# Optimization experiments

Hardware: AMD Instinct MI355X
Metric: run time of the kernel (lower is better)

## Reference

```python
import jax, jax.numpy as jnp
import numpy as np
import math

M, T, D, H, QK, K_ACT = 16, 512, 512, 512, 256, 4


def setup_inputs() -> dict:
    key = jax.random.key(0)
    ks = jax.random.split(key, 16)

    def xavier(k, shape):
        fan = shape[-1] + shape[-2]
        return jax.random.normal(k, shape, jnp.float32) * np.float32(math.sqrt(2.0 / fan))

    def bias(k, shape, fan_in):
        b = np.float32(1.0 / math.sqrt(fan_in))
        return jax.random.uniform(k, shape, jnp.float32, -b, b)

    return {
        "inputs": jax.random.normal(ks[0], (M, T, D), jnp.float32),
        # per-mechanism InputSelection params
        "Wq": xavier(ks[1], (M, QK, H)), "bq": bias(ks[2], (M, QK), H),
        "Wk": xavier(ks[3], (M, QK, D)), "bk": bias(ks[4], (M, QK), D),
        "Wv": xavier(ks[5], (M, D, D)), "bv": bias(ks[6], (M, D), D),
        # per-mechanism LSTMCell params (gate order i, f, g, o)
        "W_ih": xavier(ks[7], (M, 4 * H, D)), "b_ih": bias(ks[8], (M, 4 * H), H),
        "W_hh": xavier(ks[9], (M, 4 * H, H)), "b_hh": bias(ks[10], (M, 4 * H), H),
        # GroupLinearLayer weights for interaction attention
        "Wq_g": xavier(ks[11], (M, H, H)),
        "Wk_g": xavier(ks[12], (M, H, H)),
        "Wv_g": xavier(ks[13], (M, H, H)),
    }


def reference(inputs, Wq, bq, Wk, bk, Wv, bv, W_ih, b_ih, W_hh, b_hh, Wq_g, Wk_g, Wv_g):
    scale = 1.0 / math.sqrt(Wk.shape[1])  # 1/sqrt(key_size)
    xs = jnp.swapaxes(inputs, 0, 1)  # (T, M, D) for scan over time
    h0 = jnp.zeros((M, H), inputs.dtype)
    c0 = jnp.zeros((M, H), inputs.dtype)

    def step(carry, x_t):
        h, c = carry  # (M,H), (M,H)
        # --- InputSelection: augmented input rows are [zeros, x_t] ---
        q = jnp.einsum('mh,mqh->mq', h, Wq) + bq            # (M,QK)
        key_x = jnp.einsum('md,mkd->mk', x_t, Wk) + bk      # key of real input row
        logit0 = jnp.sum(q * bk, -1) * scale                # key of zero row == bias
        logit1 = jnp.sum(q * key_x, -1) * scale
        att = jax.nn.softmax(jnp.stack([logit0, logit1], -1), axis=-1)  # (M,2)
        val1 = jnp.einsum('md,mvd->mv', x_t, Wv) + bv       # (M,D)
        sel = att[:, 0:1] * bv + att[:, 1:2] * val1         # value of zero row == bias
        # --- top-k routing: smallest attention to the null input ---
        _, active_idx = jax.lax.top_k(-att[:, 0], K_ACT)
        mask = jnp.zeros((M,), inputs.dtype).at[active_idx].set(1.0)
        m = mask[:, None]
        # --- LSTMCell for all mechanisms, masked afterwards ---
        gates = (jnp.einsum('md,mgd->mg', sel, W_ih) + b_ih
                 + jnp.einsum('mh,mgh->mg', h, W_hh) + b_hh)  # (M,4H)
        i, f, g, o = jnp.split(gates, 4, axis=-1)
        c_new = jax.nn.sigmoid(f) * c + jax.nn.sigmoid(i) * jnp.tanh(g)
        h_new = jax.nn.sigmoid(o) * jnp.tanh(c_new)
        temp_h = m * h_new + (1 - m) * h
        new_c = m * c_new  # inactive cells are reset to zero (as in original)
        # --- interaction attention across mechanisms ---
        q2 = jnp.einsum('mh,mho->mo', temp_h, Wq_g)
        k2 = jnp.einsum('mh,mho->mo', temp_h, Wk_g)
        v2 = jnp.einsum('mh,mho->mo', temp_h, Wv_g)
        att2 = jax.nn.softmax(q2 @ k2.T, axis=1)            # (M,M), no sqrt scaling
        inter = (m * att2) @ v2                             # zero rows for inactive
        new_h = inter + (1 - m) * h + m * temp_h
        return (new_h, new_c), (new_h.reshape(-1), active_idx)

    _, (all_h, all_idx) = jax.lax.scan(step, (h0, c0), xs)
    return all_h, all_idx  # (T, M*H), (T, K_ACT)
```

## Files before the change

kernel.cpp:

```cpp
#include <hip/hip_runtime.h>

constexpr int M_ = 16, T_ = 512, D_ = 512, H_ = 512, QK_ = 256, G4_ = 2048;
constexpr float SCALE_ = 1.0f / 16.0f;

constexpr size_t KEY_OFF = 0;
constexpr size_t VAL_OFF = 2097152;
constexpr size_t H_OFF   = 6291456;
constexpr size_t C_OFF   = H_OFF + 8192;
constexpr size_t TH_OFF  = C_OFF + 8192;
constexpr size_t K2_OFF  = TH_OFF + 8192;
constexpr size_t V2_OFF  = K2_OFF + 8192;
constexpr size_t Q2_OFF  = V2_OFF + 8192;
constexpr size_t L0_OFF  = Q2_OFF + 2048;
constexpr size_t L1_OFF  = L0_OFF + 256;
constexpr size_t BAR_OFF = L1_OFF + 256;
constexpr int    BAR_WORDS = 16 * 32 + 32;

__device__ inline void load8f(const float* p, float f[8]) {
  float4 a = reinterpret_cast<const float4*>(p)[0];
  float4 b = reinterpret_cast<const float4*>(p)[1];
  f[0] = a.x; f[1] = a.y; f[2] = a.z; f[3] = a.w;
  f[4] = b.x; f[5] = b.y; f[6] = b.z; f[7] = b.w;
}

__device__ inline float waveReduce(float v) {
#pragma unroll
  for (int d = 32; d > 0; d >>= 1) v += __shfl_xor(v, d);
  return v;
}

__device__ inline float sigm(float x) { return 1.f / (1.f + expf(-x)); }

__device__ __forceinline__ void gbar(float* wsf, unsigned idx) {
  unsigned* bar = reinterpret_cast<unsigned*>(wsf + BAR_OFF);
  __syncthreads();
  if (threadIdx.x == 0) {
    __threadfence();
    const int sub = blockIdx.x >> 4;
    unsigned a = __hip_atomic_fetch_add(&bar[sub * 32], 1u, __ATOMIC_RELAXED,
                                        __HIP_MEMORY_SCOPE_AGENT);
    if (a == idx * 16u - 1u)
      __hip_atomic_fetch_add(&bar[512], 1u, __ATOMIC_RELAXED,
                             __HIP_MEMORY_SCOPE_AGENT);
    while (__hip_atomic_load(&bar[512], __ATOMIC_RELAXED,
                             __HIP_MEMORY_SCOPE_AGENT) < idx * 16u)
      __builtin_amdgcn_s_sleep(2);
    __threadfence();
  }
  __syncthreads();
}

__global__ void __launch_bounds__(256) keyval_kernel(
    const float* __restrict__ x, const float* __restrict__ Wk,
    const float* __restrict__ Wv, const float* __restrict__ bk,
    const float* __restrict__ bv, float* __restrict__ wsf) {
  __shared__ float Xs[64][33];
  __shared__ float Ws[64][33];
  int bid = blockIdx.x, tid = threadIdx.x;
  if (bid == 0) {
    for (int i = tid; i < BAR_WORDS; i += 256)
      reinterpret_cast<unsigned*>(wsf + BAR_OFF)[i] = 0u;
  }
  int m = bid / 96, r = bid % 96;
  int tt = r / 12, ot = r % 12;
  const float* xb = x + ((size_t)m * T_ + tt * 64) * D_;
  const float* wb; const float* bias; float* dst; int ld;
  if (ot < 4) {
    wb = Wk + (size_t)m * QK_ * D_ + (size_t)(ot * 64) * D_;
    bias = bk + m * QK_ + ot * 64;
    dst = wsf + KEY_OFF + ((size_t)m * T_ + tt * 64) * QK_ + ot * 64;
    ld = QK_;
  } else {
    wb = Wv + (size_t)m * D_ * D_ + (size_t)((ot - 4) * 64) * D_;
    bias = bv + m * D_ + (ot - 4) * 64;
    dst = wsf + VAL_OFF + ((size_t)m * T_ + tt * 64) * D_ + (ot - 4) * 64;
    ld = D_;
  }
  int lr = tid >> 2, lc = (tid & 3) * 8;
  int tx = tid & 15, ty = tid >> 4;
  float acc[4][4] = {};
  for (int k0 = 0; k0 < D_; k0 += 32) {
    float tmp[8];
    load8f(xb + (size_t)lr * D_ + k0 + lc, tmp);
#pragma unroll
    for (int i = 0; i < 8; ++i) Xs[lr][lc + i] = tmp[i];
    load8f(wb + (size_t)lr * D_ + k0 + lc, tmp);
#pragma unroll
    for (int i = 0; i < 8; ++i) Ws[lr][lc + i] = tmp[i];
    __syncthreads();
#pragma unroll
    for (int kk = 0; kk < 32; ++kk) {
      float xa[4], wv4[4];
#pragma unroll
      for (int a = 0; a < 4; ++a) xa[a] = Xs[ty * 4 + a][kk];
#pragma unroll
      for (int b = 0; b < 4; ++b) wv4[b] = Ws[tx * 4 + b][kk];
#pragma unroll
      for (int a = 0; a < 4; ++a)
#pragma unroll
        for (int b = 0; b < 4; ++b) acc[a][b] += xa[a] * wv4[b];
    }
    __syncthreads();
  }
#pragma unroll
  for (int b = 0; b < 4; ++b) {
    float bias_v = bias[tx * 4 + b];
#pragma unroll
    for (int a = 0; a < 4; ++a)
      dst[(size_t)(ty * 4 + a) * ld + tx * 4 + b] = acc[a][b] + bias_v;
  }
}

__global__ void __launch_bounds__(1024, 4) rim_main(
    const float* __restrict__ Wq, const float* __restrict__ bq,
    const float* __restrict__ bk, const float* __restrict__ bv,
    const float* __restrict__ Wih, const float* __restrict__ bih,
    const float* __restrict__ Whh, const float* __restrict__ bhh,
    const float* __restrict__ Wqg, const float* __restrict__ Wkg,
    const float* __restrict__ Wvg,
    float* __restrict__ wsf, float* __restrict__ out0, float* __restrict__ out1) {
  const int wg = blockIdx.x, tid = threadIdx.x;
  const int lane = tid & 63, wv = tid >> 6;
  const int m = wg >> 4, g = wg & 15;
  const int h32 = tid >> 5, oi = tid & 31;

  float* keyA = wsf + KEY_OFF;
  float* valA = wsf + VAL_OFF;
  float* hB  = wsf + H_OFF;
  float* cB  = wsf + C_OFF;
  float* thB = wsf + TH_OFF;
  float* k2B = wsf + K2_OFF;
  float* v2B = wsf + V2_OFF;
  float* q2B = wsf + Q2_OFF;
  float* l0B = wsf + L0_OFF;
  float* l1B = wsf + L1_OFF;

  __shared__ float s_newh[4][512];
  __shared__ float s_dv[512];
  __shared__ float s_pdk[16][32];
  __shared__ float s_pdv[16][32];
  __shared__ float s_pdq[16][32];
  __shared__ float s_small[64];
  __shared__ float s_w2[64];
  __shared__ float s_redA[16];
  __shared__ float s_redB[16];
  __shared__ float s_gv[4][8];

  float wqr[8], wkr[16], wvr[16];
  load8f(Wq + ((size_t)m * QK_ + g * 16 + wv) * H_ + lane * 8, wqr);
  {
    const size_t wo = ((size_t)m * H_ + h32 * 16) * H_ + g * 32 + oi;
#pragma unroll
    for (int i = 0; i < 16; ++i) wkr[i] = Wkg[wo + (size_t)i * H_];
#pragma unroll
    for (int i = 0; i < 16; ++i) wvr[i] = Wvg[wo + (size_t)i * H_];
  }
  const float qb = bq[m * QK_ + g * 16 + wv];
  const float kb = bk[m * QK_ + g * 16 + wv];

  unsigned bno = 0;

  if (g == 0 && tid < 512) {
    hB[m * 512 + tid] = 0.f;
    cB[m * 512 + tid] = 0.f;
  }
  gbar(wsf, ++bno);

  int p0 = 0, p1 = 0, p2 = 0, p3 = 0;
  int r0 = 0, r1 = 0, r2 = 0, r3 = 0;

  for (int t = 0; t <= T_; ++t) {
    int slot = -1;
    if (t > 0) {
      slot = (m == p0) ? 0 : (m == p1) ? 1 : (m == p2) ? 2 : (m == p3) ? 3 : -1;
      if (slot >= 0) {
        if (tid < 512) {
          int pr = tid >> 3, part = tid & 7;
          int s_ = pr >> 4, j_ = pr & 15;
          const float4* q4 = reinterpret_cast<const float4*>(q2B + s_ * 512 + part * 64);
          const float4* k4 = reinterpret_cast<const float4*>(k2B + j_ * 512 + part * 64);
          float acc = 0.f;
#pragma unroll
          for (int i = 0; i < 16; ++i) {
            float4 a = q4[i], b = k4[i];
            acc += a.x * b.x + a.y * b.y + a.z * b.z + a.w * b.w;
          }
          acc += __shfl_xor(acc, 1);
          acc += __shfl_xor(acc, 2);
          acc += __shfl_xor(acc, 4);
          if (part == 0) s_small[pr] = acc;
        }
        __syncthreads();
        if (tid < 4) {
          float mx = -1e30f;
          for (int j = 0; j < 16; ++j) mx = fmaxf(mx, s_small[tid * 16 + j]);
          float sm = 0.f;
          for (int j = 0; j < 16; ++j) {
            float e = expf(s_small[tid * 16 + j] - mx);
            s_w2[tid * 16 + j] = e; sm += e;
          }
          float inv = 1.f / sm;
          for (int j = 0; j < 16; ++j) s_w2[tid * 16 + j] *= inv;
        }
        __syncthreads();
        {
          int s_ = tid >> 8, o0 = (tid & 255) * 2;
          float ax = 0.f, ay = 0.f;
#pragma unroll
          for (int j = 0; j < 16; ++j) {
            float w = s_w2[s_ * 16 + j];
            float2 v = *reinterpret_cast<const float2*>(v2B + j * 512 + o0);
            ax += w * v.x; ay += w * v.y;
          }
          int myrow = s_ == 0 ? p0 : s_ == 1 ? p1 : s_ == 2 ? p2 : p3;
          const float2 th = *reinterpret_cast<const float2*>(thB + (size_t)myrow * 512 + o0);
          s_newh[s_][o0] = ax + th.x;
          s_newh[s_][o0 + 1] = ay + th.y;
        }
        __syncthreads();
      }
      if (g == 0 && tid < 512) {
        float v = (slot >= 0) ? s_newh[slot][tid] : hB[m * 512 + tid];
        out0[(size_t)(t - 1) * (M_ * H_) + m * 512 + tid] = v;
        if (slot >= 0) hB[m * 512 + tid] = v;
      }
    }
    if (t == T_) break;

    {
      float kv = keyA[((size_t)m * T_ + t) * QK_ + g * 16 + wv];
      float hreg[8];
      if (slot >= 0) {
#pragma unroll
        for (int i = 0; i < 8; ++i) hreg[i] = s_newh[slot][lane * 8 + i];
      } else {
        load8f(hB + m * 512 + lane * 8, hreg);
      }
      float acc = 0.f;
#pragma unroll
      for (int i = 0; i < 8; ++i) acc += hreg[i] * wqr[i];
      acc = waveReduce(acc);
      if (lane == 0) {
        float q = acc + qb;
        s_redA[wv] = q * kv;
        s_redB[wv] = q * kb;
      }
      __syncthreads();
      if (tid == 0) {
        float a = 0.f, b = 0.f;
        for (int w = 0; w < 16; ++w) { a += s_redA[w]; b += s_redB[w]; }
        l1B[m * 16 + g] = a;
        l0B[m * 16 + g] = b;
      }
    }
    gbar(wsf, ++bno);

    if (tid < 16) {
      float l0 = 0.f, l1 = 0.f;
      for (int i = 0; i < 16; ++i) { l0 += l0B[tid * 16 + i]; l1 += l1B[tid * 16 + i]; }
      l0 *= SCALE_; l1 *= SCALE_;
      float mx = fmaxf(l0, l1);
      float e0 = expf(l0 - mx), e1 = expf(l1 - mx);
      float inv = 1.f / (e0 + e1);
      s_small[tid] = e0 * inv;
      s_small[16 + tid] = e1 * inv;
    }
    __syncthreads();
    {
      unsigned chosen = 0;
      int rr[4];
#pragma unroll
      for (int s = 0; s < 4; ++s) {
        float best = -2.f; int bm = 0;
        for (int mm = 0; mm < 16; ++mm) {
          if (chosen & (1u << mm)) continue;
          float v = -s_small[mm];
          if (v > best) { best = v; bm = mm; }
        }
        rr[s] = bm; chosen |= 1u << bm;
      }
      r0 = rr[0]; r1 = rr[1]; r2 = rr[2]; r3 = rr[3];
    }
    if (wg == 0 && tid < 4) {
      int rowv = tid == 0 ? r0 : tid == 1 ? r1 : tid == 2 ? r2 : r3;
      out1[(size_t)t * 4 + tid] = (float)rowv;
    }
    {
      int slot_c = wg >> 6, jc = wg & 63, j0 = jc * 8;
      int mA = slot_c == 0 ? r0 : slot_c == 1 ? r1 : slot_c == 2 ? r2 : r3;
      float a0v = s_small[mA], a1v = s_small[16 + mA];
      float bvr[8], vlr[8], hr[8];
      load8f(bv + mA * D_ + lane * 8, bvr);
      load8f(valA + ((size_t)mA * T_ + t) * D_ + lane * 8, vlr);
      load8f(hB + mA * 512 + lane * 8, hr);
      float selr[8];
#pragma unroll
      for (int i = 0; i < 8; ++i) selr[i] = a0v * bvr[i] + a1v * vlr[i];
#pragma unroll
      for (int u = 0; u < 2; ++u) {
        int gl = wv * 2 + u;
        int type = gl >> 3, jj = gl & 7;
        int gidx = type * 512 + j0 + jj;
        float wi[8], wh[8];
        load8f(Wih + ((size_t)mA * G4_ + gidx) * D_ + lane * 8, wi);
        load8f(Whh + ((size_t)mA * G4_ + gidx) * H_ + lane * 8, wh);
        float acc = 0.f;
#pragma unroll
        for (int k = 0; k < 8; ++k) acc += selr[k] * wi[k] + hr[k] * wh[k];
        acc = waveReduce(acc);
        if (lane == 0)
          s_gv[type][jj] = acc + bih[mA * G4_ + gidx] + bhh[mA * G4_ + gidx];
      }
      __syncthreads();
      if (tid < 8) {
        float gi = s_gv[0][tid], gf = s_gv[1][tid], gg = s_gv[2][tid], go = s_gv[3][tid];
        int j = j0 + tid;
        float cold = cB[mA * 512 + j];
        float cn = sigm(gf) * cold + sigm(gi) * tanhf(gg);
        float hn = sigm(go) * tanhf(cn);
        cB[mA * 512 + j] = cn;
        thB[mA * 512 + j] = hn;
      }
    }
    gbar(wsf, ++bno);

    {
      unsigned amask = (1u << r0) | (1u << r1) | (1u << r2) | (1u << r3);
      unsigned pmask = (1u << p0) | (1u << p1) | (1u << p2) | (1u << p3);
      bool act = (amask >> m) & 1;
      bool prevact = (t > 0) && ((pmask >> m) & 1);
      bool dirty = act || prevact || (t == 0);
      if (dirty) {
        const float* src = act ? thB + m * 512 : hB + m * 512;
        if (tid < 512) s_dv[tid] = src[tid];
        float wq2[16];
        int qslot = -1;
        if (act) {
          qslot = (m == r0) ? 0 : (m == r1) ? 1 : (m == r2) ? 2 : 3;
          const size_t wo = ((size_t)m * H_ + h32 * 16) * H_ + g * 32 + oi;
#pragma unroll
          for (int i = 0; i < 16; ++i) wq2[i] = Wqg[wo + (size_t)i * H_];
        }
        __syncthreads();
        float pk = 0.f, pv = 0.f, pq = 0.f;
#pragma unroll
        for (int i = 0; i < 16; ++i) {
          float s = s_dv[h32 * 16 + i];
          pk += s * wkr[i];
          pv += s * wvr[i];
        }
        if (act) {
#pragma unroll
          for (int i = 0; i < 16; ++i) pq += s_dv[h32 * 16 + i] * wq2[i];
        }
        pk += __shfl_xor(pk, 32);
        pv += __shfl_xor(pv, 32);
        pq += __shfl_xor(pq, 32);
        if (lane < 32) {
          s_pdk[wv][lane] = pk;
          s_pdv[wv][lane] = pv;
          s_pdq[wv][lane] = pq;
        }
        __syncthreads();
        if (tid < 32) {
          float a = 0.f, b = 0.f, c = 0.f;
          for (int w = 0; w < 16; ++w) {
            a += s_pdk[w][tid]; b += s_pdv[w][tid]; c += s_pdq[w][tid];
          }
          k2B[m * 512 + g * 32 + tid] = a;
          v2B[m * 512 + g * 32 + tid] = b;
          if (act) q2B[qslot * 512 + g * 32 + tid] = c;
        }
      }
      if (!act && prevact && g == 0 && tid < 512) cB[m * 512 + tid] = 0.f;
    }
    p0 = r0; p1 = r1; p2 = r2; p3 = r3;
    gbar(wsf, ++bno);
  }
}

extern "C" void kernel_launch(void* const* d_in, const int* in_sizes, int n_in,
                              void* d_out, int out_size, void* d_ws, size_t ws_size,
                              hipStream_t stream) {
  const float* x   = (const float*)d_in[0];
  const float* Wq  = (const float*)d_in[1];
  const float* bq  = (const float*)d_in[2];
  const float* Wk  = (const float*)d_in[3];
  const float* bk  = (const float*)d_in[4];
  const float* Wv  = (const float*)d_in[5];
  const float* bv  = (const float*)d_in[6];
  const float* Wih = (const float*)d_in[7];
  const float* bih = (const float*)d_in[8];
  const float* Whh = (const float*)d_in[9];
  const float* bhh = (const float*)d_in[10];
  const float* Wqg = (const float*)d_in[11];
  const float* Wkg = (const float*)d_in[12];
  const float* Wvg = (const float*)d_in[13];
  float* wsf = (float*)d_ws;
  float* out0 = (float*)d_out;
  float* out1 = out0 + (size_t)T_ * M_ * H_;
  (void)in_sizes; (void)n_in; (void)out_size; (void)ws_size;

  hipLaunchKernelGGL(keyval_kernel, dim3(1536), dim3(256), 0, stream,
                     x, Wk, Wv, bk, bv, wsf);

  void* kargs[] = {(void*)&Wq, (void*)&bq, (void*)&bk, (void*)&bv,
                   (void*)&Wih, (void*)&bih, (void*)&Whh, (void*)&bhh,
                   (void*)&Wqg, (void*)&Wkg, (void*)&Wvg,
                   (void*)&wsf, (void*)&out0, (void*)&out1};
  hipLaunchCooperativeKernel((void*)rim_main, dim3(256), dim3(1024), kargs, 0,
                             stream);
}
```

Baseline: 35.69 ms.

## Replace grid barrier threadfences with agent-scope atomic loads/stores for shared state

```diff
diff --git a/kernel.cpp b/kernel.cpp
--- a/kernel.cpp
+++ b/kernel.cpp
@@ -23,6 +23,24 @@
   f[4] = b.x; f[5] = b.y; f[6] = b.z; f[7] = b.w;
 }
 
+__device__ __forceinline__ float ldf(const float* p) {
+  return __hip_atomic_load(p, __ATOMIC_RELAXED, __HIP_MEMORY_SCOPE_AGENT);
+}
+__device__ __forceinline__ void stf(float* p, float v) {
+  __hip_atomic_store(p, v, __ATOMIC_RELAXED, __HIP_MEMORY_SCOPE_AGENT);
+}
+__device__ __forceinline__ float2 ldf2(const float* p) {
+  unsigned long long u = __hip_atomic_load(
+      reinterpret_cast<const unsigned long long*>(p),
+      __ATOMIC_RELAXED, __HIP_MEMORY_SCOPE_AGENT);
+  return __builtin_bit_cast(float2, u);
+}
+__device__ __forceinline__ void ld8f_cg(const float* p, float f[8]) {
+  float2 a = ldf2(p), b = ldf2(p + 2), c = ldf2(p + 4), d = ldf2(p + 6);
+  f[0] = a.x; f[1] = a.y; f[2] = b.x; f[3] = b.y;
+  f[4] = c.x; f[5] = c.y; f[6] = d.x; f[7] = d.y;
+}
+
 __device__ inline float waveReduce(float v) {
 #pragma unroll
   for (int d = 32; d > 0; d >>= 1) v += __shfl_xor(v, d);
@@ -33,9 +51,9 @@
 
 __device__ __forceinline__ void gbar(float* wsf, unsigned idx) {
   unsigned* bar = reinterpret_cast<unsigned*>(wsf + BAR_OFF);
+  asm volatile("s_waitcnt vmcnt(0)" ::: "memory");
   __syncthreads();
   if (threadIdx.x == 0) {
-    __threadfence();
     const int sub = blockIdx.x >> 4;
     unsigned a = __hip_atomic_fetch_add(&bar[sub * 32], 1u, __ATOMIC_RELAXED,
                                         __HIP_MEMORY_SCOPE_AGENT);
@@ -44,10 +62,10 @@
                              __HIP_MEMORY_SCOPE_AGENT);
     while (__hip_atomic_load(&bar[512], __ATOMIC_RELAXED,
                              __HIP_MEMORY_SCOPE_AGENT) < idx * 16u)
-      __builtin_amdgcn_s_sleep(2);
-    __threadfence();
+      __builtin_amdgcn_s_sleep(1);
   }
   __syncthreads();
+  __builtin_amdgcn_sched_barrier(0);
 }
 
 __global__ void __launch_bounds__(256) keyval_kernel(
@@ -140,6 +158,8 @@
   __shared__ float s_pdk[16][32];
   __shared__ float s_pdv[16][32];
   __shared__ float s_pdq[16][32];
+  __shared__ float s_l0[256];
+  __shared__ float s_l1[256];
   __shared__ float s_small[64];
   __shared__ float s_w2[64];
   __shared__ float s_redA[16];
@@ -161,8 +181,8 @@
   unsigned bno = 0;
 
   if (g == 0 && tid < 512) {
-    hB[m * 512 + tid] = 0.f;
-    cB[m * 512 + tid] = 0.f;
+    stf(hB + m * 512 + tid, 0.f);
+    stf(cB + m * 512 + tid, 0.f);
   }
   gbar(wsf, ++bno);
 
@@ -177,13 +197,14 @@
         if (tid < 512) {
           int pr = tid >> 3, part = tid & 7;
           int s_ = pr >> 4, j_ = pr & 15;
-          const float4* q4 = reinterpret_cast<const float4*>(q2B + s_ * 512 + part * 64);
-          const float4* k4 = reinterpret_cast<const float4*>(k2B + j_ * 512 + part * 64);
+          const float* q4 = q2B + s_ * 512 + part * 64;
+          const float* k4 = k2B + j_ * 512 + part * 64;
           float acc = 0.f;
 #pragma unroll
           for (int i = 0; i < 16; ++i) {
-            float4 a = q4[i], b = k4[i];
-            acc += a.x * b.x + a.y * b.y + a.z * b.z + a.w * b.w;
+            float2 a0 = ldf2(q4 + i * 4), a1 = ldf2(q4 + i * 4 + 2);
+            float2 b0 = ldf2(k4 + i * 4), b1 = ldf2(k4 + i * 4 + 2);
+            acc += a0.x * b0.x + a0.y * b0.y + a1.x * b1.x + a1.y * b1.y;
           }
           acc += __shfl_xor(acc, 1);
           acc += __shfl_xor(acc, 2);
@@ -209,20 +230,20 @@
 #pragma unroll
           for (int j = 0; j < 16; ++j) {
             float w = s_w2[s_ * 16 + j];
-            float2 v = *reinterpret_cast<const float2*>(v2B + j * 512 + o0);
+            float2 v = ldf2(v2B + j * 512 + o0);
             ax += w * v.x; ay += w * v.y;
           }
           int myrow = s_ == 0 ? p0 : s_ == 1 ? p1 : s_ == 2 ? p2 : p3;
-          const float2 th = *reinterpret_cast<const float2*>(thB + (size_t)myrow * 512 + o0);
+          float2 th = ldf2(thB + (size_t)myrow * 512 + o0);
           s_newh[s_][o0] = ax + th.x;
           s_newh[s_][o0 + 1] = ay + th.y;
         }
         __syncthreads();
       }
       if (g == 0 && tid < 512) {
-        float v = (slot >= 0) ? s_newh[slot][tid] : hB[m * 512 + tid];
+        float v = (slot >= 0) ? s_newh[slot][tid] : ldf(hB + m * 512 + tid);
         out0[(size_t)(t - 1) * (M_ * H_) + m * 512 + tid] = v;
-        if (slot >= 0) hB[m * 512 + tid] = v;
+        if (slot >= 0) stf(hB + m * 512 + tid, v);
       }
     }
     if (t == T_) break;
@@ -234,7 +255,7 @@
 #pragma unroll
         for (int i = 0; i < 8; ++i) hreg[i] = s_newh[slot][lane * 8 + i];
       } else {
-        load8f(hB + m * 512 + lane * 8, hreg);
+        ld8f_cg(hB + m * 512 + lane * 8, hreg);
       }
       float acc = 0.f;
 #pragma unroll
@@ -249,15 +270,20 @@
       if (tid == 0) {
         float a = 0.f, b = 0.f;
         for (int w = 0; w < 16; ++w) { a += s_redA[w]; b += s_redB[w]; }
-        l1B[m * 16 + g] = a;
-        l0B[m * 16 + g] = b;
+        stf(l1B + m * 16 + g, a);
+        stf(l0B + m * 16 + g, b);
       }
     }
     gbar(wsf, ++bno);
 
+    if (tid < 256) {
+      s_l0[tid] = ldf(l0B + tid);
+      s_l1[tid] = ldf(l1B + tid);
+    }
+    __syncthreads();
     if (tid < 16) {
       float l0 = 0.f, l1 = 0.f;
-      for (int i = 0; i < 16; ++i) { l0 += l0B[tid * 16 + i]; l1 += l1B[tid * 16 + i]; }
+      for (int i = 0; i < 16; ++i) { l0 += s_l0[tid * 16 + i]; l1 += s_l1[tid * 16 + i]; }
       l0 *= SCALE_; l1 *= SCALE_;
       float mx = fmaxf(l0, l1);
       float e0 = expf(l0 - mx), e1 = expf(l1 - mx);
@@ -292,7 +318,7 @@
       float bvr[8], vlr[8], hr[8];
       load8f(bv + mA * D_ + lane * 8, bvr);
       load8f(valA + ((size_t)mA * T_ + t) * D_ + lane * 8, vlr);
-      load8f(hB + mA * 512 + lane * 8, hr);
+      ld8f_cg(hB + mA * 512 + lane * 8, hr);
       float selr[8];
 #pragma unroll
       for (int i = 0; i < 8; ++i) selr[i] = a0v * bvr[i] + a1v * vlr[i];
@@ -315,11 +341,11 @@
       if (tid < 8) {
         float gi = s_gv[0][tid], gf = s_gv[1][tid], gg = s_gv[2][tid], go = s_gv[3][tid];
         int j = j0 + tid;
-        float cold = cB[mA * 512 + j];
+        float cold = ldf(cB + mA * 512 + j);
         float cn = sigm(gf) * cold + sigm(gi) * tanhf(gg);
         float hn = sigm(go) * tanhf(cn);
-        cB[mA * 512 + j] = cn;
-        thB[mA * 512 + j] = hn;
+        stf(cB + mA * 512 + j, cn);
+        stf(thB + mA * 512 + j, hn);
       }
     }
     gbar(wsf, ++bno);
@@ -332,7 +358,7 @@
       bool dirty = act || prevact || (t == 0);
       if (dirty) {
         const float* src = act ? thB + m * 512 : hB + m * 512;
-        if (tid < 512) s_dv[tid] = src[tid];
+        if (tid < 512) s_dv[tid] = ldf(src + tid);
         float wq2[16];
         int qslot = -1;
         if (act) {
@@ -367,12 +393,12 @@
           for (int w = 0; w < 16; ++w) {
             a += s_pdk[w][tid]; b += s_pdv[w][tid]; c += s_pdq[w][tid];
           }
-          k2B[m * 512 + g * 32 + tid] = a;
-          v2B[m * 512 + g * 32 + tid] = b;
-          if (act) q2B[qslot * 512 + g * 32 + tid] = c;
-        }
-      }
-      if (!act && prevact && g == 0 && tid < 512) cB[m * 512 + tid] = 0.f;
+          stf(k2B + m * 512 + g * 32 + tid, a);
+          stf(v2B + m * 512 + g * 32 + tid, b);
+          if (act) stf(q2B + qslot * 512 + g * 32 + tid, c);
+        }
+      }
+      if (!act && prevact && g == 0 && tid < 512) stf(cB + m * 512 + tid, 0.f);
     }
     p0 = r0; p1 = r1; p2 = r2; p3 = r3;
     gbar(wsf, ++bno);
```

Result: faster. 30.27 ms (-15.2%).
